# Optimization experiments

Measured on AMD Instinct MI355X. Metric: run time of the kernel, lower is better.

Reference implementation:

```python
import jax, jax.numpy as jnp
import numpy as np

B, INF, OUTF, SEQ, FUT = 128, 64, 16, 512, 96
H, L = 512, 2
PROJ = INF - OUTF  # proj_size = 48 (PyTorch LSTM proj_size semantics)


def _cell(x, h, c, Wih, Whh, bih, bhh, Whr):
    # One LSTM-with-projection step; PyTorch gate order: i, f, g, o
    gates = x @ Wih.T + h @ Whh.T + bih + bhh  # (B, 4H)
    i, f, g, o = jnp.split(gates, 4, axis=-1)
    c = jax.nn.sigmoid(f) * c + jax.nn.sigmoid(i) * jnp.tanh(g)
    h = (jax.nn.sigmoid(o) * jnp.tanh(c)) @ Whr.T  # projected hidden (B, PROJ)
    return h, c


def _run_layer(xs, p):
    # xs: (T, B, F) time-major; returns (T, B, PROJ), final (h, c)
    Wih, Whh, bih, bhh, Whr = p
    bsz = xs.shape[1]
    h0 = jnp.zeros((bsz, PROJ), xs.dtype)
    c0 = jnp.zeros((bsz, H), xs.dtype)
    def step(carry, x_t):
        h, c = carry
        h, c = _cell(x_t, h, c, Wih, Whh, bih, bhh, Whr)
        return (h, c), h
    (hT, cT), hs = jax.lax.scan(step, (h0, c0), xs)
    return hs, hT, cT


def _encoder(x_btf, layers):
    xs = jnp.swapaxes(x_btf, 0, 1)  # (T, B, INF)
    hTs, cTs = [], []
    for p in layers:
        xs, hT, cT = _run_layer(xs, p)
        hTs.append(hT); cTs.append(cT)
    return jnp.swapaxes(xs, 0, 1), tuple(hTs), tuple(cTs)


def _decoder(h0s, c0s, first_prev, dec_btf, layers):
    xs = jnp.swapaxes(dec_btf, 0, 1)  # (FUT, B, OUTF)
    def step(carry, x_t):
        hs, cs, prev = carry
        inp = jnp.concatenate([prev, x_t], axis=-1)  # (B, INF)
        nh, nc = [], []
        for l, p in enumerate(layers):
            h, c = _cell(inp, hs[l], cs[l], *p)
            nh.append(h); nc.append(c)
            inp = h
        return (tuple(nh), tuple(nc), inp), inp
    _, preds = jax.lax.scan(step, (h0s, c0s, first_prev), xs)
    return jnp.swapaxes(preds, 0, 1)  # (B, FUT, PROJ)


def _forward(theta, insample_x_t, outsample_x_t, enc_layers, dec_layers):
    x = jnp.transpose(insample_x_t, (0, 2, 1))      # (B, SEQ, INF)
    dec = jnp.transpose(outsample_x_t, (0, 2, 1))   # (B, FUT, OUTF)
    backcast_seq, hTs, cTs = _encoder(x, enc_layers)  # (B, SEQ, PROJ)
    first_prev = x[:, -1, :PROJ]  # input_elements[:, -1, :-OUTF]
    preds = _decoder(hTs, cTs, first_prev, dec, dec_layers)  # (B, FUT, PROJ)
    backcast_basis = jnp.transpose(backcast_seq, (0, 2, 1))  # (B, PROJ, SEQ)
    forecast_basis = jnp.transpose(preds, (0, 2, 1))         # (B, PROJ, FUT)
    cut = forecast_basis.shape[1]
    backcast = jnp.einsum('bp,bpt->bt', theta[:, cut:], backcast_basis)
    forecast = jnp.einsum('bp,bpt->bt', theta[:, :cut], forecast_basis)
    return backcast, forecast


def setup_inputs() -> dict:
    key = jax.random.key(0)
    ks = iter(jax.random.split(key, 64))
    s = 1.0 / float(np.sqrt(H))
    def u(shape):
        return jax.random.uniform(next(ks), shape, jnp.float32, -s, s)
    inp = {
        "theta": jax.random.normal(next(ks), (B, 2 * PROJ), jnp.float32),
        "insample_x_t": jax.random.normal(next(ks), (B, INF, SEQ), jnp.float32),
        "outsample_x_t": jax.random.normal(next(ks), (B, OUTF, FUT), jnp.float32),
    }
    for net in ("enc", "dec"):
        for l in range(L):
            in_dim = INF if l == 0 else PROJ
            inp[f"{net}_Wih{l}"] = u((4 * H, in_dim))
            inp[f"{net}_Whh{l}"] = u((4 * H, PROJ))
            inp[f"{net}_bih{l}"] = u((4 * H,))
            inp[f"{net}_bhh{l}"] = u((4 * H,))
            inp[f"{net}_Whr{l}"] = u((PROJ, H))
    return inp


def reference(theta, insample_x_t, outsample_x_t,
              enc_Wih0, enc_Whh0, enc_bih0, enc_bhh0, enc_Whr0,
              enc_Wih1, enc_Whh1, enc_bih1, enc_bhh1, enc_Whr1,
              dec_Wih0, dec_Whh0, dec_bih0, dec_bhh0, dec_Whr0,
              dec_Wih1, dec_Whh1, dec_bih1, dec_bhh1, dec_Whr1):
    enc_layers = [(enc_Wih0, enc_Whh0, enc_bih0, enc_bhh0, enc_Whr0),
                  (enc_Wih1, enc_Whh1, enc_bih1, enc_bhh1, enc_Whr1)]
    dec_layers = [(dec_Wih0, dec_Whh0, dec_bih0, dec_bhh0, dec_Whr0),
                  (dec_Wih1, dec_Whh1, dec_bih1, dec_bhh1, dec_Whr1)]
    return _forward(theta, insample_x_t, outsample_x_t, enc_layers, dec_layers)
```

## Files before the change

### kernel.cpp

```cpp
#include <hip/hip_runtime.h>
#include <cstdint>
#include <cstddef>

#define BATCH 128
#define INF   64
#define OUTF  16
#define SEQ   512
#define FUT   96
#define HID   512
#define G4    2048
#define PROJ  48
#define ECH   4

#define DRG 8
#define DBG 8
#define DUP 64
#define DBP 16

typedef float f32x4 __attribute__((ext_vector_type(4)));

__device__ __forceinline__ float fsigmoid(float x) {
    float e = __builtin_amdgcn_exp2f(-1.4426950408889634f * x);
    return __builtin_amdgcn_rcpf(1.0f + e);
}
__device__ __forceinline__ float ftanh(float x) {
    float e = __builtin_amdgcn_exp2f(2.8853900817779268f * x);
    return 1.0f - 2.0f * __builtin_amdgcn_rcpf(1.0f + e);
}

__device__ __forceinline__ float gload(const float* p) {
    return __hip_atomic_load(p, __ATOMIC_RELAXED, __HIP_MEMORY_SCOPE_AGENT);
}
__device__ __forceinline__ void gstore(float* p, float v) {
    __hip_atomic_store(p, v, __ATOMIC_RELAXED, __HIP_MEMORY_SCOPE_AGENT);
}

__device__ __forceinline__ f32x4 gsum8(const float* p, size_t stride) {
    f32x4 a0, a1, a2, a3, a4, a5, a6, a7;
    asm volatile(
        "global_load_dwordx4 %0, %8, off sc0 sc1\n\t"
        "global_load_dwordx4 %1, %9, off sc0 sc1\n\t"
        "global_load_dwordx4 %2, %10, off sc0 sc1\n\t"
        "global_load_dwordx4 %3, %11, off sc0 sc1\n\t"
        "global_load_dwordx4 %4, %12, off sc0 sc1\n\t"
        "global_load_dwordx4 %5, %13, off sc0 sc1\n\t"
        "global_load_dwordx4 %6, %14, off sc0 sc1\n\t"
        "global_load_dwordx4 %7, %15, off sc0 sc1\n\t"
        "s_waitcnt vmcnt(0)"
        : "=&v"(a0), "=&v"(a1), "=&v"(a2), "=&v"(a3),
          "=&v"(a4), "=&v"(a5), "=&v"(a6), "=&v"(a7)
        : "v"(p), "v"(p + stride), "v"(p + 2 * stride), "v"(p + 3 * stride),
          "v"(p + 4 * stride), "v"(p + 5 * stride), "v"(p + 6 * stride),
          "v"(p + 7 * stride)
        : "memory");
    return ((a0 + a1) + (a2 + a3)) + ((a4 + a5) + (a6 + a7));
}

__device__ __forceinline__ void bsync(unsigned* ctr, unsigned target, int tid) {
    asm volatile("s_waitcnt vmcnt(0)" ::: "memory");
    __syncthreads();
    if (tid == 0) {
        __hip_atomic_fetch_add(ctr, 1u, __ATOMIC_RELAXED, __HIP_MEMORY_SCOPE_AGENT);
        while (__hip_atomic_load(ctr, __ATOMIC_RELAXED, __HIP_MEMORY_SCOPE_AGENT) < target)
            __builtin_amdgcn_s_sleep(2);
    }
    __syncthreads();
    asm volatile("" ::: "memory");
}

__global__ void k_wtrans(const float* __restrict__ W, float* __restrict__ WT,
                         int R, int C) {
    __shared__ float tile[32][33];
    int r0 = blockIdx.x * 32, c0 = blockIdx.y * 32;
    int tx = threadIdx.x, ty = threadIdx.y;
    #pragma unroll
    for (int i = 0; i < 4; ++i) {
        int r = r0 + ty + 8 * i;
        if (r < R && c0 + tx < C) tile[ty + 8 * i][tx] = W[(size_t)r * C + c0 + tx];
    }
    __syncthreads();
    #pragma unroll
    for (int i = 0; i < 4; ++i) {
        int c = c0 + ty + 8 * i;
        if (c < C && r0 + tx < R) WT[(size_t)c * R + r0 + tx] = tile[tx][ty + 8 * i];
    }
}

__global__ __launch_bounds__(512) void k_enc(
    const float* __restrict__ x,
    const float* __restrict__ WT0, const float* __restrict__ Whh0,
    const float* __restrict__ bih0, const float* __restrict__ bhh0,
    const float* __restrict__ Whr0,
    const float* __restrict__ WT1, const float* __restrict__ Whh1,
    const float* __restrict__ bih1, const float* __restrict__ bhh1,
    const float* __restrict__ Whr1,
    float* __restrict__ H0x, float* __restrict__ H1,
    float* __restrict__ hs, float* __restrict__ cs,
    unsigned* __restrict__ eflags)
{
    const bool L1w = blockIdx.x >= BATCH;
    const int b = L1w ? blockIdx.x - BATCH : blockIdx.x;
    const int j = threadIdx.x;
    const int wave = j >> 6, lane = j & 63;
    const float* WT  = L1w ? WT1 : WT0;
    const float* Whh = L1w ? Whh1 : Whh0;
    const float* Whr = L1w ? Whr1 : Whr0;
    const float* bih = L1w ? bih1 : bih0;
    const float* bhh = L1w ? bhh1 : bhh0;
    const int K = L1w ? PROJ : INF;

    __shared__ float whr[PROJ][HID + 4];
    __shared__ __align__(16) float xs[ECH][INF + 4];
    __shared__ __align__(16) float ht_lds[HID];
    __shared__ __align__(16) float h_cur[PROJ];

    float wI[PROJ], wF[PROJ], wG[PROJ], wO[PROJ];
    #pragma unroll
    for (int k4 = 0; k4 < 12; ++k4) {
        float4 vi = *reinterpret_cast<const float4*>(&Whh[(size_t)j * PROJ + 4 * k4]);
        float4 vf = *reinterpret_cast<const float4*>(&Whh[(size_t)(j + HID) * PROJ + 4 * k4]);
        float4 vg = *reinterpret_cast<const float4*>(&Whh[(size_t)(j + 2 * HID) * PROJ + 4 * k4]);
        float4 vo = *reinterpret_cast<const float4*>(&Whh[(size_t)(j + 3 * HID) * PROJ + 4 * k4]);
        wI[4*k4+0]=vi.x; wI[4*k4+1]=vi.y; wI[4*k4+2]=vi.z; wI[4*k4+3]=vi.w;
        wF[4*k4+0]=vf.x; wF[4*k4+1]=vf.y; wF[4*k4+2]=vf.z; wF[4*k4+3]=vf.w;
        wG[4*k4+0]=vg.x; wG[4*k4+1]=vg.y; wG[4*k4+2]=vg.z; wG[4*k4+3]=vg.w;
        wO[4*k4+0]=vo.x; wO[4*k4+1]=vo.y; wO[4*k4+2]=vo.z; wO[4*k4+3]=vo.w;
    }
    for (int idx = j; idx < PROJ * HID; idx += 512) {
        int p = idx >> 9, jj = idx & 511;
        whr[p][jj] = Whr[(size_t)p * HID + jj];
    }
    float bI = bih[j] + bhh[j];
    float bF = bih[j + HID] + bhh[j + HID];
    float bG = bih[j + 2 * HID] + bhh[j + 2 * HID];
    float bO = bih[j + 3 * HID] + bhh[j + 3 * HID];
    float c = 0.f;
    if (j < PROJ) h_cur[j] = 0.f;
    __syncthreads();

    for (int t0 = 0; t0 < SEQ; t0 += ECH) {
        if (!L1w) {
            if (j < INF * ECH) {
                int k = j >> 2, dt = j & 3;
                xs[dt][k] = x[(size_t)b * INF * SEQ + (size_t)k * SEQ + t0 + dt];
            }
        } else {
            if (j == 0) {
                unsigned need = (unsigned)(t0 / ECH) + 1;
                while (__hip_atomic_load(&eflags[b * 16], __ATOMIC_RELAXED,
                                         __HIP_MEMORY_SCOPE_AGENT) < need)
                    __builtin_amdgcn_s_sleep(2);
            }
            __syncthreads();
            asm volatile("" ::: "memory");
            if (j < PROJ * ECH) {
                int dt = j / PROJ, p = j % PROJ;
                xs[dt][p] = gload(&H0x[((size_t)(t0 + dt) * BATCH + b) * PROJ + p]);
            }
        }
        __syncthreads();

        float a0[ECH], a1[ECH], a2[ECH], a3[ECH];
        #pragma unroll
        for (int dt = 0; dt < ECH; ++dt) { a0[dt] = bI; a1[dt] = bF; }
        for (int kq = 0; kq < K / 4; ++kq) {
            float wi0 = WT[(size_t)(kq*4+0) * G4 + j];
            float wi1 = WT[(size_t)(kq*4+1) * G4 + j];
            float wi2 = WT[(size_t)(kq*4+2) * G4 + j];
            float wi3 = WT[(size_t)(kq*4+3) * G4 + j];
            float wf0 = WT[(size_t)(kq*4+0) * G4 + HID + j];
            float wf1 = WT[(size_t)(kq*4+1) * G4 + HID + j];
            float wf2 = WT[(size_t)(kq*4+2) * G4 + HID + j];
            float wf3 = WT[(size_t)(kq*4+3) * G4 + HID + j];
            #pragma unroll
            for (int dt = 0; dt < ECH; ++dt) {
                float4 xv = *reinterpret_cast<const float4*>(&xs[dt][kq * 4]);
                a0[dt] += wi0*xv.x + wi1*xv.y + wi2*xv.z + wi3*xv.w;
                a1[dt] += wf0*xv.x + wf1*xv.y + wf2*xv.z + wf3*xv.w;
            }
        }
        #pragma unroll
        for (int dt = 0; dt < ECH; ++dt) { a2[dt] = bG; a3[dt] = bO; }
        for (int kq = 0; kq < K / 4; ++kq) {
            float wg0 = WT[(size_t)(kq*4+0) * G4 + 2 * HID + j];
            float wg1 = WT[(size_t)(kq*4+1) * G4 + 2 * HID + j];
            float wg2 = WT[(size_t)(kq*4+2) * G4 + 2 * HID + j];
            float wg3 = WT[(size_t)(kq*4+3) * G4 + 2 * HID + j];
            float wo0 = WT[(size_t)(kq*4+0) * G4 + 3 * HID + j];
            float wo1 = WT[(size_t)(kq*4+1) * G4 + 3 * HID + j];
            float wo2 = WT[(size_t)(kq*4+2) * G4 + 3 * HID + j];
            float wo3 = WT[(size_t)(kq*4+3) * G4 + 3 * HID + j];
            #pragma unroll
            for (int dt = 0; dt < ECH; ++dt) {
                float4 xv = *reinterpret_cast<const float4*>(&xs[dt][kq * 4]);
                a2[dt] += wg0*xv.x + wg1*xv.y + wg2*xv.z + wg3*xv.w;
                a3[dt] += wo0*xv.x + wo1*xv.y + wo2*xv.z + wo3*xv.w;
            }
        }

        #pragma unroll
        for (int dt = 0; dt < ECH; ++dt) {
            float ai = a0[dt], af = a1[dt], ag = a2[dt], ao = a3[dt];
            #pragma unroll
            for (int k4 = 0; k4 < 12; ++k4) {
                float4 h4 = *reinterpret_cast<const float4*>(&h_cur[4 * k4]);
                ai += wI[4*k4+0]*h4.x + wI[4*k4+1]*h4.y + wI[4*k4+2]*h4.z + wI[4*k4+3]*h4.w;
                af += wF[4*k4+0]*h4.x + wF[4*k4+1]*h4.y + wF[4*k4+2]*h4.z + wF[4*k4+3]*h4.w;
                ag += wG[4*k4+0]*h4.x + wG[4*k4+1]*h4.y + wG[4*k4+2]*h4.z + wG[4*k4+3]*h4.w;
                ao += wO[4*k4+0]*h4.x + wO[4*k4+1]*h4.y + wO[4*k4+2]*h4.z + wO[4*k4+3]*h4.w;
            }
            float si = fsigmoid(ai), sf = fsigmoid(af), so = fsigmoid(ao), tg = ftanh(ag);
            c = sf * c + si * tg;
            ht_lds[j] = so * ftanh(c);
            __syncthreads();
            float rq[6];
            #pragma unroll
            for (int q = 0; q < 6; ++q) {
                int p = wave * 6 + q;
                float s = 0.f;
                #pragma unroll
                for (int m = 0; m < 8; ++m)
                    s += whr[p][lane + 64 * m] * ht_lds[lane + 64 * m];
                #pragma unroll
                for (int o = 32; o; o >>= 1) s += __shfl_xor(s, o, 64);
                rq[q] = s;
            }
            if (lane == 0) {
                int t = t0 + dt;
                #pragma unroll
                for (int q = 0; q < 6; ++q) {
                    int p = wave * 6 + q;
                    float v = rq[q];
                    h_cur[p] = v;
                    if (!L1w) gstore(&H0x[((size_t)t * BATCH + b) * PROJ + p], v);
                    else      H1[((size_t)t * BATCH + b) * PROJ + p] = v;
                }
            }
            __syncthreads();
        }
        if (!L1w) {
            asm volatile("s_waitcnt vmcnt(0)" ::: "memory");
            __syncthreads();
            if (j == 0)
                __hip_atomic_store(&eflags[b * 16], (unsigned)(t0 / ECH) + 1,
                                   __ATOMIC_RELAXED, __HIP_MEMORY_SCOPE_AGENT);
        }
    }
    cs[((size_t)(L1w ? BATCH : 0) + b) * HID + j] = c;
    if (j < PROJ) hs[((size_t)(L1w ? BATCH : 0) + b) * PROJ + j] = h_cur[j];
}

__global__ __launch_bounds__(512) void k_decP(
    const float* __restrict__ xdec,
    const float* __restrict__ Wih0, const float* __restrict__ Whh0,
    const float* __restrict__ bih0, const float* __restrict__ bhh0,
    const float* __restrict__ Whr0,
    const float* __restrict__ Wih1, const float* __restrict__ Whh1,
    const float* __restrict__ bih1, const float* __restrict__ bhh1,
    const float* __restrict__ Whr1,
    const float* __restrict__ hs, const float* __restrict__ cs,
    const float* __restrict__ xin,
    float* __restrict__ PPa,
    float* __restrict__ PPb,
    float* __restrict__ PRED,
    unsigned* __restrict__ bar)
{
    const int bg = blockIdx.x & 7, rg = blockIdx.x >> 3;
    const int tid = threadIdx.x;
    const int kq = tid & 3, rhalf = tid >> 2;
    const int u2 = tid >> 3, b2 = tid & 7;
    const int uglob = rg * DUP + u2;
    const int w = tid >> 6, lane = tid & 63;
    const size_t PSTR = (size_t)BATCH * PROJ;
    const size_t DPP  = (size_t)DRG * PSTR;

    __shared__ __align__(16) float inp0[DBP][120];
    __shared__ __align__(16) float h1b[DBP][52];
    __shared__ __align__(16) float h0n[DBP][52];
    __shared__ float xch[4][DUP][17];
    __shared__ float htl[DBP][68];
    __shared__ float wslT0[DUP][52];
    __shared__ float wslT1[DUP][52];

    for (int i = tid; i < PROJ * DUP; i += 512) {
        int p = i >> 6, uu = i & 63;
        wslT0[uu][p] = Whr0[(size_t)p * HID + rg * DUP + uu];
        wslT1[uu][p] = Whr1[(size_t)p * HID + rg * DUP + uu];
    }
    float bs0[4], bs1[4];
    #pragma unroll
    for (int gg = 0; gg < 4; ++gg) {
        bs0[gg] = bih0[gg * HID + uglob] + bhh0[gg * HID + uglob];
        bs1[gg] = bih1[gg * HID + uglob] + bhh1[gg * HID + uglob];
    }
    float c0[2], c1[2];
    #pragma unroll
    for (int hh = 0; hh < 2; ++hh) {
        int bglob = bg * DBP + b2 + 8 * hh;
        c0[hh] = cs[(size_t)bglob * HID + uglob];
        c1[hh] = cs[(size_t)(BATCH + bglob) * HID + uglob];
    }
    __syncthreads();

    unsigned* ctr = bar + bg * 64;
    unsigned phase = 0;

    for (int t = 0; t < FUT; ++t) {
        const float* ppaR = PPa + (size_t)((t - 1) & 1) * DPP;
        float*       ppaW = PPa + (size_t)(t & 1) * DPP;
        const float* ppbR = PPb + (size_t)((t - 1) & 1) * DPP;
        float*       ppbW = PPb + (size_t)(t & 1) * DPP;

        if (t == 0) {
            for (int i = tid; i < DBP * PROJ; i += 512) {
                int b = i / PROJ, p = i % PROJ;
                int bglob = bg * DBP + b;
                inp0[b][p]      = hs[(size_t)bglob * PROJ + p];
                inp0[b][48 + p] = xin[(size_t)bglob * INF * SEQ + (size_t)p * SEQ + (SEQ - 1)];
                h1b[b][p]       = hs[(size_t)(BATCH + bglob) * PROJ + p];
            }
            if (tid < DBP * OUTF) {
                int b = tid >> 4, f = tid & 15;
                inp0[b][96 + f] = xdec[(size_t)(bg * DBP + b) * (OUTF * FUT) + (size_t)f * FUT];
            }
        } else {
            if (tid < 192) {
                int b = tid / 12, p = (tid % 12) * 4;
                int bglob = bg * DBP + b;
                f32x4 s = gsum8(ppaR + (size_t)bglob * PROJ + p, PSTR);
                *reinterpret_cast<f32x4*>(&inp0[b][p]) = s;
            } else if (tid < 384) {
                int idx = tid - 192;
                int b = idx / 12, p = (idx % 12) * 4;
                int bglob = bg * DBP + b;
                f32x4 s = gsum8(ppbR + (size_t)bglob * PROJ + p, PSTR);
                *reinterpret_cast<f32x4*>(&inp0[b][48 + p]) = s;
                *reinterpret_cast<f32x4*>(&h1b[b][p]) = s;
                if (rg == 0)
                    *reinterpret_cast<f32x4*>(&PRED[((size_t)(t - 1) * BATCH + bglob) * PROJ + p]) = s;
            } else {
                #pragma unroll
                for (int rep = 0; rep < 2; ++rep) {
                    int i2 = (tid - 384) + rep * 128;
                    int b = i2 >> 4, f = i2 & 15;
                    inp0[b][96 + f] = xdec[(size_t)(bg * DBP + b) * (OUTF * FUT) + (size_t)f * FUT + t];
                }
            }
        }
        __syncthreads();

        #pragma unroll
        for (int p = 0; p < 2; ++p) {
            int rid = p * 128 + rhalf;
            int g = rid >> 6, u = rid & 63;
            int grow = g * HID + rg * DUP + u;
            float wv[28];
            #pragma unroll
            for (int kk = 0; kk < 28; ++kk) {
                int k = kq * 28 + kk;
                wv[kk] = (k < 48) ? Whh0[(size_t)grow * 48 + k]
                                  : Wih0[(size_t)grow * 64 + (k - 48)];
            }
            float acc[DBP];
            #pragma unroll
            for (int b = 0; b < DBP; ++b) acc[b] = 0.f;
            const float* srcA = &inp0[0][0] + kq * 28;
            #pragma unroll
            for (int i4 = 0; i4 < 7; ++i4) {
                float w0 = wv[i4*4], w1 = wv[i4*4+1], w2 = wv[i4*4+2], w3 = wv[i4*4+3];
                #pragma unroll
                for (int b = 0; b < DBP; ++b) {
                    float4 xv = *reinterpret_cast<const float4*>(&srcA[b * 120 + i4 * 4]);
                    acc[b] += w0*xv.x + w1*xv.y + w2*xv.z + w3*xv.w;
                }
            }
            #pragma unroll
            for (int b = 0; b < DBP; ++b) {
                acc[b] += __shfl_xor(acc[b], 1, 64);
                acc[b] += __shfl_xor(acc[b], 2, 64);
            }
            if (kq == 0) {
                #pragma unroll
                for (int b = 0; b < DBP; ++b) xch[g][u][b] = acc[b];
            }
        }
        __syncthreads();
        #pragma unroll
        for (int hh = 0; hh < 2; ++hh) {
            int b = b2 + 8 * hh;
            float gi = xch[0][u2][b] + bs0[0];
            float gf = xch[1][u2][b] + bs0[1];
            float gc = xch[2][u2][b] + bs0[2];
            float go = xch[3][u2][b] + bs0[3];
            float si = fsigmoid(gi), sf = fsigmoid(gf), so = fsigmoid(go), tg = ftanh(gc);
            c0[hh] = sf * c0[hh] + si * tg;
            htl[b][u2] = so * ftanh(c0[hh]);
        }
        __syncthreads();
        if (lane < PROJ) {
            #pragma unroll
            for (int bb = 0; bb < 2; ++bb) {
                int b = 2 * w + bb;
                float s = 0.f;
                #pragma unroll
                for (int u4 = 0; u4 < 16; ++u4) {
                    float4 hv = *reinterpret_cast<const float4*>(&htl[b][u4 * 4]);
                    s += wslT0[u4*4+0][lane]*hv.x + wslT0[u4*4+1][lane]*hv.y
                       + wslT0[u4*4+2][lane]*hv.z + wslT0[u4*4+3][lane]*hv.w;
                }
                gstore(&ppaW[(size_t)rg * PSTR + (size_t)(bg * DBP + b) * PROJ + lane], s);
            }
        }
        phase += 1;
        bsync(ctr, phase * DRG, tid);

        if (tid < 192) {
            int b = tid / 12, p = (tid % 12) * 4;
            f32x4 s = gsum8(ppaW + (size_t)(bg * DBP + b) * PROJ + p, PSTR);
            *reinterpret_cast<f32x4*>(&h0n[b][p]) = s;
        }
        __syncthreads();

        #pragma unroll
        for (int p = 0; p < 2; ++p) {
            int rid = p * 128 + rhalf;
            int g = rid >> 6, u = rid & 63;
            int grow = g * HID + rg * DUP + u;
            float wv[24];
            #pragma unroll
            for (int kk = 0; kk < 24; ++kk) {
                int k = kq * 24 + kk;
                wv[kk] = (k < 48) ? Whh1[(size_t)grow * 48 + k]
                                  : Wih1[(size_t)grow * 48 + (k - 48)];
            }
            const float* srcB = (kq < 2) ? (&h1b[0][0] + kq * 24)
                                         : (&h0n[0][0] + (kq - 2) * 24);
            float acc[DBP];
            #pragma unroll
            for (int b = 0; b < DBP; ++b) acc[b] = 0.f;
            #pragma unroll
            for (int i4 = 0; i4 < 6; ++i4) {
                float w0 = wv[i4*4], w1 = wv[i4*4+1], w2 = wv[i4*4+2], w3 = wv[i4*4+3];
                #pragma unroll
                for (int b = 0; b < DBP; ++b) {
                    float4 xv = *reinterpret_cast<const float4*>(&srcB[b * 52 + i4 * 4]);
                    acc[b] += w0*xv.x + w1*xv.y + w2*xv.z + w3*xv.w;
                }
            }
            #pragma unroll
            for (int b = 0; b < DBP; ++b) {
                acc[b] += __shfl_xor(acc[b], 1, 64);
                acc[b] += __shfl_xor(acc[b], 2, 64);
            }
            if (kq == 0) {
                #pragma unroll
                for (int b = 0; b < DBP; ++b) xch[g][u][b] = acc[b];
            }
        }
        __syncthreads();
        #pragma unroll
        for (int hh = 0; hh < 2; ++hh) {
            int b = b2 + 8 * hh;
            float gi = xch[0][u2][b] + bs1[0];
            float gf = xch[1][u2][b] + bs1[1];
            float gc = xch[2][u2][b] + bs1[2];
            float go = xch[3][u2][b] + bs1[3];
            float si = fsigmoid(gi), sf = fsigmoid(gf), so = fsigmoid(go), tg = ftanh(gc);
            c1[hh] = sf * c1[hh] + si * tg;
            htl[b][u2] = so * ftanh(c1[hh]);
        }
        __syncthreads();
        if (lane < PROJ) {
            #pragma unroll
            for (int bb = 0; bb < 2; ++bb) {
                int b = 2 * w + bb;
                float s = 0.f;
                #pragma unroll
                for (int u4 = 0; u4 < 16; ++u4) {
                    float4 hv = *reinterpret_cast<const float4*>(&htl[b][u4 * 4]);
                    s += wslT1[u4*4+0][lane]*hv.x + wslT1[u4*4+1][lane]*hv.y
                       + wslT1[u4*4+2][lane]*hv.z + wslT1[u4*4+3][lane]*hv.w;
                }
                gstore(&ppbW[(size_t)rg * PSTR + (size_t)(bg * DBP + b) * PROJ + lane], s);
            }
        }
        phase += 1;
        bsync(ctr, phase * DRG, tid);
    }

    if (tid < 2 * PROJ) {
        int bb = tid / PROJ, p = tid % PROJ;
        int bglob = bg * DBP + 2 * rg + bb;
        const float* ppbF = PPb + (size_t)((FUT - 1) & 1) * DPP;
        float s = 0.f;
        #pragma unroll
        for (int rr = 0; rr < DRG; ++rr)
            s += gload(&ppbF[(size_t)rr * PSTR + (size_t)bglob * PROJ + p]);
        PRED[((size_t)(FUT - 1) * BATCH + bglob) * PROJ + p] = s;
    }
}

__global__ void k_final(const float* __restrict__ theta, const float* __restrict__ H1,
                        const float* __restrict__ PRED, float* __restrict__ out)
{
    int b = blockIdx.x;
    __shared__ float th[2 * PROJ];
    if (threadIdx.x < 2 * PROJ) th[threadIdx.x] = theta[(size_t)b * 2 * PROJ + threadIdx.x];
    __syncthreads();
    for (int t = threadIdx.x; t < SEQ; t += 256) {
        float s = 0.f;
        #pragma unroll
        for (int p = 0; p < PROJ; ++p) s += th[PROJ + p] * H1[((size_t)t * BATCH + b) * PROJ + p];
        out[(size_t)b * SEQ + t] = s;
    }
    for (int t = threadIdx.x; t < FUT; t += 256) {
        float s = 0.f;
        #pragma unroll
        for (int p = 0; p < PROJ; ++p) s += th[p] * PRED[((size_t)t * BATCH + b) * PROJ + p];
        out[(size_t)BATCH * SEQ + (size_t)b * FUT + t] = s;
    }
}

extern "C" void kernel_launch(void* const* d_in, const int* in_sizes, int n_in,
                              void* d_out, int out_size, void* d_ws, size_t ws_size,
                              hipStream_t stream)
{
    (void)in_sizes; (void)n_in; (void)out_size; (void)ws_size;
    const float* theta = (const float*)d_in[0];
    const float* xin   = (const float*)d_in[1];
    const float* xdec  = (const float*)d_in[2];
    const float* eW0i = (const float*)d_in[3];
    const float* eW0h = (const float*)d_in[4];
    const float* eb0i = (const float*)d_in[5];
    const float* eb0h = (const float*)d_in[6];
    const float* eW0r = (const float*)d_in[7];
    const float* eW1i = (const float*)d_in[8];
    const float* eW1h = (const float*)d_in[9];
    const float* eb1i = (const float*)d_in[10];
    const float* eb1h = (const float*)d_in[11];
    const float* eW1r = (const float*)d_in[12];
    const float* dW0i = (const float*)d_in[13];
    const float* dW0h = (const float*)d_in[14];
    const float* db0i = (const float*)d_in[15];
    const float* db0h = (const float*)d_in[16];
    const float* dW0r = (const float*)d_in[17];
    const float* dW1i = (const float*)d_in[18];
    const float* dW1h = (const float*)d_in[19];
    const float* db1i = (const float*)d_in[20];
    const float* db1h = (const float*)d_in[21];
    const float* dW1r = (const float*)d_in[22];

    float* ws = (float*)d_ws;
    size_t off = 0;
    float* H0x  = ws + off; off += (size_t)SEQ * BATCH * PROJ;
    float* H1   = ws + off; off += (size_t)SEQ * BATCH * PROJ;
    float* PRED = ws + off; off += (size_t)FUT * BATCH * PROJ;
    float* hs   = ws + off; off += (size_t)2 * BATCH * PROJ;
    float* cs   = ws + off; off += (size_t)2 * BATCH * HID;
    float* WT0  = ws + off; off += (size_t)INF * G4;
    float* WT1  = ws + off; off += (size_t)PROJ * G4;
    const size_t DPP = (size_t)DRG * BATCH * PROJ;
    float* PPa  = ws + off; off += 2 * DPP;
    float* PPb  = ws + off; off += 2 * DPP;
    off = (off + 63) & ~(size_t)63;
    unsigned* eflags = (unsigned*)(ws + off); off += BATCH * 16;
    unsigned* bar    = (unsigned*)(ws + off); off += DBG * 64;

    hipMemsetAsync(eflags, 0, (BATCH * 16 + DBG * 64) * sizeof(unsigned), stream);
    k_wtrans<<<dim3(G4 / 32, 2), dim3(32, 8), 0, stream>>>(eW0i, WT0, G4, INF);
    k_wtrans<<<dim3(G4 / 32, 2), dim3(32, 8), 0, stream>>>(eW1i, WT1, G4, PROJ);
    k_enc<<<2 * BATCH, 512, 0, stream>>>(xin,
                                         WT0, eW0h, eb0i, eb0h, eW0r,
                                         WT1, eW1h, eb1i, eb1h, eW1r,
                                         H0x, H1, hs, cs, eflags);
    k_decP<<<DRG * DBG, 512, 0, stream>>>(xdec, dW0i, dW0h, db0i, db0h, dW0r,
                                          dW1i, dW1h, db1i, db1h, dW1r,
                                          hs, cs, xin, PPa, PPb, PRED, bar);
    k_final<<<BATCH, 256, 0, stream>>>(theta, H1, PRED, (float*)d_out);
}
```

Measured before the change: 4.996 ms.

## Store encoder input and recurrent weights in fp16, stream Whh from memory

```diff
diff --git a/kernel.cpp b/kernel.cpp
--- a/kernel.cpp
+++ b/kernel.cpp
@@ -1,4 +1,5 @@
 #include <hip/hip_runtime.h>
+#include <hip/hip_fp16.h>
 #include <cstdint>
 #include <cstddef>
 
@@ -68,30 +69,26 @@
     asm volatile("" ::: "memory");
 }
 
-__global__ void k_wtrans(const float* __restrict__ W, float* __restrict__ WT,
-                         int R, int C) {
-    __shared__ float tile[32][33];
-    int r0 = blockIdx.x * 32, c0 = blockIdx.y * 32;
-    int tx = threadIdx.x, ty = threadIdx.y;
-    #pragma unroll
-    for (int i = 0; i < 4; ++i) {
-        int r = r0 + ty + 8 * i;
-        if (r < R && c0 + tx < C) tile[ty + 8 * i][tx] = W[(size_t)r * C + c0 + tx];
-    }
-    __syncthreads();
-    #pragma unroll
-    for (int i = 0; i < 4; ++i) {
-        int c = c0 + ty + 8 * i;
-        if (c < C && r0 + tx < R) WT[(size_t)c * R + r0 + tx] = tile[tx][ty + 8 * i];
-    }
+__global__ void k_wtrans16(const float* __restrict__ W, uint32_t* __restrict__ WT16p, int K) {
+    int idx = blockIdx.x * 256 + threadIdx.x;
+    if (idx >= (K / 2) * G4) return;
+    int row = idx & (G4 - 1);
+    int kp  = idx >> 11;
+    __half2 p = __halves2half2(__float2half(W[(size_t)row * K + 2 * kp]),
+                               __float2half(W[(size_t)row * K + 2 * kp + 1]));
+    WT16p[idx] = *reinterpret_cast<uint32_t*>(&p);
+}
+__global__ void k_cvt16(const float* __restrict__ W, __half* __restrict__ H, int n) {
+    int i = blockIdx.x * 256 + threadIdx.x;
+    if (i < n) H[i] = __float2half(W[i]);
 }
 
 __global__ __launch_bounds__(512) void k_enc(
     const float* __restrict__ x,
-    const float* __restrict__ WT0, const float* __restrict__ Whh0,
+    const uint32_t* __restrict__ WT16_0, const __half* __restrict__ Whh16_0,
     const float* __restrict__ bih0, const float* __restrict__ bhh0,
     const float* __restrict__ Whr0,
-    const float* __restrict__ WT1, const float* __restrict__ Whh1,
+    const uint32_t* __restrict__ WT16_1, const __half* __restrict__ Whh16_1,
     const float* __restrict__ bih1, const float* __restrict__ bhh1,
     const float* __restrict__ Whr1,
     float* __restrict__ H0x, float* __restrict__ H1,
@@ -102,8 +99,8 @@
     const int b = L1w ? blockIdx.x - BATCH : blockIdx.x;
     const int j = threadIdx.x;
     const int wave = j >> 6, lane = j & 63;
-    const float* WT  = L1w ? WT1 : WT0;
-    const float* Whh = L1w ? Whh1 : Whh0;
+    const uint32_t* WT16 = L1w ? WT16_1 : WT16_0;
+    const __half* Whh16  = L1w ? Whh16_1 : Whh16_0;
     const float* Whr = L1w ? Whr1 : Whr0;
     const float* bih = L1w ? bih1 : bih0;
     const float* bhh = L1w ? bhh1 : bhh0;
@@ -114,18 +111,6 @@
     __shared__ __align__(16) float ht_lds[HID];
     __shared__ __align__(16) float h_cur[PROJ];
 
-    float wI[PROJ], wF[PROJ], wG[PROJ], wO[PROJ];
-    #pragma unroll
-    for (int k4 = 0; k4 < 12; ++k4) {
-        float4 vi = *reinterpret_cast<const float4*>(&Whh[(size_t)j * PROJ + 4 * k4]);
-        float4 vf = *reinterpret_cast<const float4*>(&Whh[(size_t)(j + HID) * PROJ + 4 * k4]);
-        float4 vg = *reinterpret_cast<const float4*>(&Whh[(size_t)(j + 2 * HID) * PROJ + 4 * k4]);
-        float4 vo = *reinterpret_cast<const float4*>(&Whh[(size_t)(j + 3 * HID) * PROJ + 4 * k4]);
-        wI[4*k4+0]=vi.x; wI[4*k4+1]=vi.y; wI[4*k4+2]=vi.z; wI[4*k4+3]=vi.w;
-        wF[4*k4+0]=vf.x; wF[4*k4+1]=vf.y; wF[4*k4+2]=vf.z; wF[4*k4+3]=vf.w;
-        wG[4*k4+0]=vg.x; wG[4*k4+1]=vg.y; wG[4*k4+2]=vg.z; wG[4*k4+3]=vg.w;
-        wO[4*k4+0]=vo.x; wO[4*k4+1]=vo.y; wO[4*k4+2]=vo.z; wO[4*k4+3]=vo.w;
-    }
     for (int idx = j; idx < PROJ * HID; idx += 512) {
         int p = idx >> 9, jj = idx & 511;
         whr[p][jj] = Whr[(size_t)p * HID + jj];
@@ -138,6 +123,11 @@
     if (j < PROJ) h_cur[j] = 0.f;
     __syncthreads();
 
+    const __half* whI = Whh16 + (size_t)j * PROJ;
+    const __half* whF = Whh16 + (size_t)(j + HID) * PROJ;
+    const __half* whG = Whh16 + (size_t)(j + 2 * HID) * PROJ;
+    const __half* whO = Whh16 + (size_t)(j + 3 * HID) * PROJ;
+
     for (int t0 = 0; t0 < SEQ; t0 += ECH) {
         if (!L1w) {
             if (j < INF * ECH) {
@@ -164,37 +154,41 @@
         #pragma unroll
         for (int dt = 0; dt < ECH; ++dt) { a0[dt] = bI; a1[dt] = bF; }
         for (int kq = 0; kq < K / 4; ++kq) {
-            float wi0 = WT[(size_t)(kq*4+0) * G4 + j];
-            float wi1 = WT[(size_t)(kq*4+1) * G4 + j];
-            float wi2 = WT[(size_t)(kq*4+2) * G4 + j];
-            float wi3 = WT[(size_t)(kq*4+3) * G4 + j];
-            float wf0 = WT[(size_t)(kq*4+0) * G4 + HID + j];
-            float wf1 = WT[(size_t)(kq*4+1) * G4 + HID + j];
-            float wf2 = WT[(size_t)(kq*4+2) * G4 + HID + j];
-            float wf3 = WT[(size_t)(kq*4+3) * G4 + HID + j];
+            uint32_t di0 = WT16[(size_t)(kq * 2 + 0) * G4 + j];
+            uint32_t di1 = WT16[(size_t)(kq * 2 + 1) * G4 + j];
+            uint32_t df0 = WT16[(size_t)(kq * 2 + 0) * G4 + HID + j];
+            uint32_t df1 = WT16[(size_t)(kq * 2 + 1) * G4 + HID + j];
+            const __half* hi0 = (const __half*)&di0;
+            const __half* hi1 = (const __half*)&di1;
+            const __half* hf0 = (const __half*)&df0;
+            const __half* hf1 = (const __half*)&df1;
             #pragma unroll
             for (int dt = 0; dt < ECH; ++dt) {
                 float4 xv = *reinterpret_cast<const float4*>(&xs[dt][kq * 4]);
-                a0[dt] += wi0*xv.x + wi1*xv.y + wi2*xv.z + wi3*xv.w;
-                a1[dt] += wf0*xv.x + wf1*xv.y + wf2*xv.z + wf3*xv.w;
+                a0[dt] += __half2float(hi0[0])*xv.x + __half2float(hi0[1])*xv.y
+                        + __half2float(hi1[0])*xv.z + __half2float(hi1[1])*xv.w;
+                a1[dt] += __half2float(hf0[0])*xv.x + __half2float(hf0[1])*xv.y
+                        + __half2float(hf1[0])*xv.z + __half2float(hf1[1])*xv.w;
             }
         }
         #pragma unroll
         for (int dt = 0; dt < ECH; ++dt) { a2[dt] = bG; a3[dt] = bO; }
         for (int kq = 0; kq < K / 4; ++kq) {
-            float wg0 = WT[(size_t)(kq*4+0) * G4 + 2 * HID + j];
-            float wg1 = WT[(size_t)(kq*4+1) * G4 + 2 * HID + j];
-            float wg2 = WT[(size_t)(kq*4+2) * G4 + 2 * HID + j];
-            float wg3 = WT[(size_t)(kq*4+3) * G4 + 2 * HID + j];
-            float wo0 = WT[(size_t)(kq*4+0) * G4 + 3 * HID + j];
-            float wo1 = WT[(size_t)(kq*4+1) * G4 + 3 * HID + j];
-            float wo2 = WT[(size_t)(kq*4+2) * G4 + 3 * HID + j];
-            float wo3 = WT[(size_t)(kq*4+3) * G4 + 3 * HID + j];
+            uint32_t dg0 = WT16[(size_t)(kq * 2 + 0) * G4 + 2 * HID + j];
+            uint32_t dg1 = WT16[(size_t)(kq * 2 + 1) * G4 + 2 * HID + j];
+            uint32_t do0 = WT16[(size_t)(kq * 2 + 0) * G4 + 3 * HID + j];
+            uint32_t do1 = WT16[(size_t)(kq * 2 + 1) * G4 + 3 * HID + j];
+            const __half* hg0 = (const __half*)&dg0;
+            const __half* hg1 = (const __half*)&dg1;
+            const __half* ho0 = (const __half*)&do0;
+            const __half* ho1 = (const __half*)&do1;
             #pragma unroll
             for (int dt = 0; dt < ECH; ++dt) {
                 float4 xv = *reinterpret_cast<const float4*>(&xs[dt][kq * 4]);
-                a2[dt] += wg0*xv.x + wg1*xv.y + wg2*xv.z + wg3*xv.w;
-                a3[dt] += wo0*xv.x + wo1*xv.y + wo2*xv.z + wo3*xv.w;
+                a2[dt] += __half2float(hg0[0])*xv.x + __half2float(hg0[1])*xv.y
+                        + __half2float(hg1[0])*xv.z + __half2float(hg1[1])*xv.w;
+                a3[dt] += __half2float(ho0[0])*xv.x + __half2float(ho0[1])*xv.y
+                        + __half2float(ho1[0])*xv.z + __half2float(ho1[1])*xv.w;
             }
         }
 
@@ -203,11 +197,23 @@
             float ai = a0[dt], af = a1[dt], ag = a2[dt], ao = a3[dt];
             #pragma unroll
             for (int k4 = 0; k4 < 12; ++k4) {
+                float2 rI = *reinterpret_cast<const float2*>(whI + 4 * k4);
+                float2 rF = *reinterpret_cast<const float2*>(whF + 4 * k4);
+                float2 rG = *reinterpret_cast<const float2*>(whG + 4 * k4);
+                float2 rO = *reinterpret_cast<const float2*>(whO + 4 * k4);
+                const __half* hI = (const __half*)&rI;
+                const __half* hF = (const __half*)&rF;
+                const __half* hG = (const __half*)&rG;
+                const __half* hO = (const __half*)&rO;
                 float4 h4 = *reinterpret_cast<const float4*>(&h_cur[4 * k4]);
-                ai += wI[4*k4+0]*h4.x + wI[4*k4+1]*h4.y + wI[4*k4+2]*h4.z + wI[4*k4+3]*h4.w;
-                af += wF[4*k4+0]*h4.x + wF[4*k4+1]*h4.y + wF[4*k4+2]*h4.z + wF[4*k4+3]*h4.w;
-                ag += wG[4*k4+0]*h4.x + wG[4*k4+1]*h4.y + wG[4*k4+2]*h4.z + wG[4*k4+3]*h4.w;
-                ao += wO[4*k4+0]*h4.x + wO[4*k4+1]*h4.y + wO[4*k4+2]*h4.z + wO[4*k4+3]*h4.w;
+                ai += __half2float(hI[0])*h4.x + __half2float(hI[1])*h4.y
+                    + __half2float(hI[2])*h4.z + __half2float(hI[3])*h4.w;
+                af += __half2float(hF[0])*h4.x + __half2float(hF[1])*h4.y
+                    + __half2float(hF[2])*h4.z + __half2float(hF[3])*h4.w;
+                ag += __half2float(hG[0])*h4.x + __half2float(hG[1])*h4.y
+                    + __half2float(hG[2])*h4.z + __half2float(hG[3])*h4.w;
+                ao += __half2float(hO[0])*h4.x + __half2float(hO[1])*h4.y
+                    + __half2float(hO[2])*h4.z + __half2float(hO[3])*h4.w;
             }
             float si = fsigmoid(ai), sf = fsigmoid(af), so = fsigmoid(ao), tg = ftanh(ag);
             c = sf * c + si * tg;
@@ -260,8 +266,7 @@
     const float* __restrict__ Whr1,
     const float* __restrict__ hs, const float* __restrict__ cs,
     const float* __restrict__ xin,
-    float* __restrict__ PPa,
-    float* __restrict__ PPb,
+    float* __restrict__ PPa, float* __restrict__ PPb,
     float* __restrict__ PRED,
     unsigned* __restrict__ bar)
 {
@@ -557,8 +562,10 @@
     float* PRED = ws + off; off += (size_t)FUT * BATCH * PROJ;
     float* hs   = ws + off; off += (size_t)2 * BATCH * PROJ;
     float* cs   = ws + off; off += (size_t)2 * BATCH * HID;
-    float* WT0  = ws + off; off += (size_t)INF * G4;
-    float* WT1  = ws + off; off += (size_t)PROJ * G4;
+    uint32_t* WT16_0 = (uint32_t*)(ws + off); off += (size_t)(INF / 2) * G4;
+    uint32_t* WT16_1 = (uint32_t*)(ws + off); off += (size_t)(PROJ / 2) * G4;
+    __half* Whh16_0  = (__half*)(ws + off);   off += (size_t)G4 * PROJ / 2;
+    __half* Whh16_1  = (__half*)(ws + off);   off += (size_t)G4 * PROJ / 2;
     const size_t DPP = (size_t)DRG * BATCH * PROJ;
     float* PPa  = ws + off; off += 2 * DPP;
     float* PPb  = ws + off; off += 2 * DPP;
@@ -567,11 +574,13 @@
     unsigned* bar    = (unsigned*)(ws + off); off += DBG * 64;
 
     hipMemsetAsync(eflags, 0, (BATCH * 16 + DBG * 64) * sizeof(unsigned), stream);
-    k_wtrans<<<dim3(G4 / 32, 2), dim3(32, 8), 0, stream>>>(eW0i, WT0, G4, INF);
-    k_wtrans<<<dim3(G4 / 32, 2), dim3(32, 8), 0, stream>>>(eW1i, WT1, G4, PROJ);
+    k_wtrans16<<<((INF / 2) * G4 + 255) / 256, 256, 0, stream>>>(eW0i, WT16_0, INF);
+    k_wtrans16<<<((PROJ / 2) * G4 + 255) / 256, 256, 0, stream>>>(eW1i, WT16_1, PROJ);
+    k_cvt16<<<(G4 * PROJ + 255) / 256, 256, 0, stream>>>(eW0h, Whh16_0, G4 * PROJ);
+    k_cvt16<<<(G4 * PROJ + 255) / 256, 256, 0, stream>>>(eW1h, Whh16_1, G4 * PROJ);
     k_enc<<<2 * BATCH, 512, 0, stream>>>(xin,
-                                         WT0, eW0h, eb0i, eb0h, eW0r,
-                                         WT1, eW1h, eb1i, eb1h, eW1r,
+                                         WT16_0, Whh16_0, eb0i, eb0h, eW0r,
+                                         WT16_1, Whh16_1, eb1i, eb1h, eW1r,
                                          H0x, H1, hs, cs, eflags);
     k_decP<<<DRG * DBG, 512, 0, stream>>>(xdec, dW0i, dW0h, db0i, db0h, dW0r,
                                           dW1i, dW1h, db1i, db1h, dW1r,
```

New measurement: 7.534 ms. +50.8%, slower.
